# Performance work log

Hardware: AMD Instinct MI355X
Metric: run time of the kernel (lower is better)

Reference implementation:

```python
import jax, jax.numpy as jnp
import numpy as np

B = 131072
HID = 512
TEMB = 32
N_STEPS = 10


def time_embedding(t):
    # t: (B,) -> (B, TEMB) sinusoidal embedding
    half = TEMB // 2
    freqs = jnp.exp(-jnp.log(10000.0) * jnp.arange(half, dtype=jnp.float32) / half)
    args = t[:, None] * freqs[None, :]
    return jnp.concatenate([jnp.sin(args), jnp.cos(args)], axis=-1)


def setup_inputs() -> dict:
    key = jax.random.key(0)
    ks = jax.random.split(key, 9)
    def lin(k, fan_out, fan_in):
        s = 1.0 / np.sqrt(fan_in)
        kw, kb = jax.random.split(k)
        W = jax.random.uniform(kw, (fan_out, fan_in), jnp.float32, -s, s)
        b = jax.random.uniform(kb, (fan_out,), jnp.float32, -s, s)
        return W, b
    x = jax.random.normal(ks[0], (B, 2), jnp.float32)
    W0, b0 = lin(ks[1], HID, 2 + TEMB)
    W1, b1 = lin(ks[2], HID, HID)
    W2, b2 = lin(ks[3], HID, HID)
    # NOTE: original zero-inits last layer (trivial flow); use small random
    # weights so the Jacobian/log-det math is exercised non-trivially.
    W3 = 0.1 * jax.random.normal(ks[4], (2, HID), jnp.float32) / np.sqrt(HID)
    b3 = jnp.zeros((2,), jnp.float32)
    return {"x": x, "W0": W0, "b0": b0, "W1": W1, "b1": b1,
            "W2": W2, "b2": b2, "W3": W3, "b3": b3}


def reference(x, W0, b0, W1, b1, W2, b2, W3, b3):
    h_step = 1.0 / N_STEPS
    nb = x.shape[0]

    def vel(z, t):
        # z: (B,2), t: (B,) -> v: (B,2)
        h = jnp.concatenate([z, time_embedding(t)], axis=-1)
        h = jax.nn.silu(h @ W0.T + b0)
        h = jax.nn.silu(h @ W1.T + b1)
        h = jax.nn.silu(h @ W2.T + b2)
        return h @ W3.T + b3

    e0 = jnp.broadcast_to(jnp.array([1.0, 0.0], jnp.float32), (nb, 2))
    e1 = jnp.broadcast_to(jnp.array([0.0, 1.0], jnp.float32), (nb, 2))

    def step(carry, k):
        z, log_det = carry
        t = jnp.full((nb,), k * h_step, jnp.float32)
        f = lambda zz: vel(zz, t)
        # Batched JVPs give Jacobian columns: col0 = dv/dz0, col1 = dv/dz1
        v, col0 = jax.jvp(f, (z,), (e0,))
        _, col1 = jax.jvp(f, (z,), (e1,))
        det = (1.0 + h_step * col0[:, 0]) * (1.0 + h_step * col1[:, 1]) \
              - (h_step ** 2) * col1[:, 0] * col0[:, 1]
        log_det = log_det + jnp.log(jnp.clip(jnp.abs(det), 1e-8))
        z = z + h_step * v
        return (z, log_det), None

    ks = jnp.arange(N_STEPS, dtype=jnp.float32)
    (z, log_det), _ = jax.lax.scan(step, (x, jnp.zeros((nb,), jnp.float32)), ks)
    log_pz = -0.5 * jnp.sum(z ** 2 + jnp.log(2.0 * jnp.pi), axis=-1)
    return log_pz + log_det
```

## Files before the change

kernel.cpp:

```cpp
#include <hip/hip_runtime.h>
#include <hip/hip_bf16.h>
#include <math.h>


typedef float  f32x4  __attribute__((ext_vector_type(4)));
typedef float  f32x16 __attribute__((ext_vector_type(16)));
typedef __bf16 bf16x8 __attribute__((ext_vector_type(8)));

#define ROWB(r) (((r) << 10) + ((r) << 4))

static __device__ __forceinline__ unsigned pkbf2(float a, float b) {
    unsigned short lo = __builtin_bit_cast(unsigned short, __float2bfloat16(a));
    unsigned short hi = __builtin_bit_cast(unsigned short, __float2bfloat16(b));
    return (unsigned)lo | ((unsigned)hi << 16);
}

__global__ void pack_w_kernel(const float* __restrict__ W,
                              __hip_bfloat16* __restrict__ out) {
    int i  = blockIdx.x * 512 + threadIdx.x;
    int c  = i >> 13;
    int nb = (i >> 9) & 15;
    int l  = (i >> 3) & 63;
    int j  = i & 7;
    int n  = nb * 32 + (l & 31);
    int k  = c * 16 + ((l >> 5) << 3) + j;
    out[i] = __float2bfloat16(W[n * 512 + k]);
}

__global__ void pack_w0_kernel(const float* __restrict__ W0,
                               float* __restrict__ w01) {
    int o = threadIdx.x;
    w01[o * 2 + 0] = W0[o * 34 + 0];
    w01[o * 2 + 1] = W0[o * 34 + 1];
}

__global__ void cstep_kernel(const float* __restrict__ W0,
                             const float* __restrict__ b0,
                             float* __restrict__ cst) {
    int k = blockIdx.x;
    int o = threadIdx.x;
    float t = (float)k * 0.1f;
    float acc = b0[o];
    #pragma unroll
    for (int j = 0; j < 16; ++j) {
        float f   = expf(-9.210340371976184f * (float)j / 16.0f);
        float arg = t * f;
        acc += W0[o * 34 + 2 + j]  * sinf(arg);
        acc += W0[o * 34 + 18 + j] * cosf(arg);
    }
    cst[k * 512 + o] = acc;
}

__global__ __launch_bounds__(1024)
void flow_kernel(const float* __restrict__ x,
                 const float* __restrict__ w01,
                 const float* __restrict__ cst,
                 const __hip_bfloat16* __restrict__ Wpk1,
                 const __hip_bfloat16* __restrict__ Wpk2,
                 const float* __restrict__ b1,
                 const float* __restrict__ b2,
                 const float* __restrict__ W3,
                 const float* __restrict__ b3v,
                 float* __restrict__ out)
{
    __shared__ __align__(16) char Xbuf[96 * 1040];
    __shared__ float zbuf[32][2];
    __shared__ float ldbuf[32];
    __shared__ __align__(16) float part[16][32][8];

    const int tid  = threadIdx.x;
    const int lane = tid & 63;
    const int wid  = tid >> 6;
    const int l31  = lane & 31;
    const int hi   = lane >> 5;
    const int n0w  = wid << 5;
    const int wgs  = blockIdx.x << 5;

    if (tid < 32) {
        zbuf[tid][0] = x[(wgs + tid) * 2 + 0];
        zbuf[tid][1] = x[(wgs + tid) * 2 + 1];
        ldbuf[tid]   = 0.0f;
    }

    const int rowb0 = ROWB(l31);
    const int rowb1 = ROWB(32 + l31);
    const int rowb2 = ROWB(64 + l31);
    const int hi16  = hi << 4;
    const int abase = (wid << 6) + lane;
    const uint4* Wp1 = (const uint4*)Wpk1;
    const uint4* Wp2 = (const uint4*)Wpk2;

    const int s0   = tid >> 5;
    const int t32  = tid & 31;

    const char* xb = (const char*)Xbuf;

    __syncthreads();

    #pragma unroll 1
    for (int step = 0; step < 10; ++step) {
        {
            const float z0 = zbuf[s0][0];
            const float z1 = zbuf[s0][1];
            const float* cs = cst + (step << 9);
            char* base0 = Xbuf + ROWB(s0);
            #pragma unroll 1
            for (int m = 0; m < 2; ++m) {
                int ob = (t32 << 4) + (m << 3);
                const float4* wv4 = (const float4*)(w01 + (ob << 1));
                const float4* cv4 = (const float4*)(cs + ob);
                unsigned ph[4], p0[4], p1[4];
                #pragma unroll
                for (int jj = 0; jj < 4; ++jj) {
                    float4 wv = wv4[jj];
                    float4 cv = cv4[jj >> 1];
                    float c0 = (jj & 1) ? cv.z : cv.x;
                    float c1 = (jj & 1) ? cv.w : cv.y;
                    float a0  = fmaf(z0, wv.x, fmaf(z1, wv.y, c0));
                    float sg0 = 1.0f / (1.0f + __expf(-a0));
                    float h0  = a0 * sg0;
                    float sp0 = fmaf(h0, 1.0f - sg0, sg0);
                    float a1  = fmaf(z0, wv.z, fmaf(z1, wv.w, c1));
                    float sg1 = 1.0f / (1.0f + __expf(-a1));
                    float h1  = a1 * sg1;
                    float sp1 = fmaf(h1, 1.0f - sg1, sg1);
                    ph[jj] = pkbf2(h0, h1);
                    p0[jj] = pkbf2(sp0 * wv.x, sp1 * wv.z);
                    p1[jj] = pkbf2(sp0 * wv.y, sp1 * wv.w);
                }
                int off = ob << 1;
                uint4 vph = {ph[0], ph[1], ph[2], ph[3]};
                uint4 vp0 = {p0[0], p0[1], p0[2], p0[3]};
                uint4 vp1 = {p1[0], p1[1], p1[2], p1[3]};
                *(uint4*)(base0 + off)             = vph;
                *(uint4*)(base0 + ROWB(32) + off)  = vp0;
                *(uint4*)(base0 + ROWB(64) + off)  = vp1;
            }
        }
        __syncthreads();

        #pragma unroll 1
        for (int layer = 0; layer < 2; ++layer) {
            const uint4* __restrict__ Wp   = layer ? Wp2 : Wp1;
            const float* __restrict__ bias = layer ? b2  : b1;

            f32x16 acc0 = (f32x16)(0.0f);
            f32x16 acc1 = (f32x16)(0.0f);
            f32x16 acc2 = (f32x16)(0.0f);

            uint4 aCur = Wp[abase];
            #pragma unroll 2
            for (int c = 0; c < 32; ++c) {
                uint4 aNxt = Wp[abase + (((c + 1) & 31) << 10)];
                int kx = (c << 5) | hi16;
                bf16x8 bf0 = __builtin_bit_cast(bf16x8, *(const uint4*)(xb + rowb0 + kx));
                bf16x8 bf1 = __builtin_bit_cast(bf16x8, *(const uint4*)(xb + rowb1 + kx));
                bf16x8 bf2 = __builtin_bit_cast(bf16x8, *(const uint4*)(xb + rowb2 + kx));
                bf16x8 av  = __builtin_bit_cast(bf16x8, aCur);
                __builtin_amdgcn_s_setprio(1);
                acc0 = __builtin_amdgcn_mfma_f32_32x32x16_bf16(av, bf0, acc0, 0, 0, 0);
                acc1 = __builtin_amdgcn_mfma_f32_32x32x16_bf16(av, bf1, acc1, 0, 0, 0);
                acc2 = __builtin_amdgcn_mfma_f32_32x32x16_bf16(av, bf2, acc2, 0, 0, 0);
                __builtin_amdgcn_s_setprio(0);
                aCur = aNxt;
            }

            if (layer == 0) {
                __syncthreads();
                char* pb = Xbuf + ROWB(l31);
                #pragma unroll
                for (int q = 0; q < 4; ++q) {
                    int nq = n0w + 8 * q + 4 * hi;
                    f32x4 bq = *(const f32x4*)(bias + nq);
                    float hv[4], u0v[4], u1v[4];
                    #pragma unroll
                    for (int k = 0; k < 4; ++k) {
                        int reg = 4 * q + k;
                        float aa  = acc0[reg] + bq[k];
                        float sig = 1.0f / (1.0f + __expf(-aa));
                        float h   = aa * sig;
                        float sp  = fmaf(h, 1.0f - sig, sig);
                        hv[k]  = h;
                        u0v[k] = sp * acc1[reg];
                        u1v[k] = sp * acc2[reg];
                    }
                    int off = nq << 1;
                    uint2 vh = {pkbf2(hv[0],  hv[1]),  pkbf2(hv[2],  hv[3])};
                    uint2 v0 = {pkbf2(u0v[0], u0v[1]), pkbf2(u0v[2], u0v[3])};
                    uint2 v1 = {pkbf2(u1v[0], u1v[1]), pkbf2(u1v[2], u1v[3])};
                    *(uint2*)(pb + off)            = vh;
                    *(uint2*)(pb + ROWB(32) + off) = v0;
                    *(uint2*)(pb + ROWB(64) + off) = v1;
                }
                __syncthreads();
            } else {
                float q0 = 0.f, q1 = 0.f, q2 = 0.f, q3 = 0.f, q4 = 0.f, q5 = 0.f;
                #pragma unroll
                for (int q = 0; q < 4; ++q) {
                    int nq = n0w + 8 * q + 4 * hi;
                    f32x4 bq = *(const f32x4*)(bias + nq);
                    f32x4 w0 = *(const f32x4*)(W3 + nq);
                    f32x4 w1 = *(const f32x4*)(W3 + 512 + nq);
                    #pragma unroll
                    for (int k = 0; k < 4; ++k) {
                        int reg = 4 * q + k;
                        float aa  = acc0[reg] + bq[k];
                        float sig = 1.0f / (1.0f + __expf(-aa));
                        float h   = aa * sig;
                        float sp  = fmaf(h, 1.0f - sig, sig);
                        float u0  = sp * acc1[reg];
                        float u1  = sp * acc2[reg];
                        q0 = fmaf(w0[k], h,  q0);
                        q1 = fmaf(w1[k], h,  q1);
                        q2 = fmaf(w0[k], u0, q2);
                        q3 = fmaf(w1[k], u0, q3);
                        q4 = fmaf(w0[k], u1, q4);
                        q5 = fmaf(w1[k], u1, q5);
                    }
                }
                q0 += __shfl_xor(q0, 32);
                q1 += __shfl_xor(q1, 32);
                q2 += __shfl_xor(q2, 32);
                q3 += __shfl_xor(q3, 32);
                q4 += __shfl_xor(q4, 32);
                q5 += __shfl_xor(q5, 32);
                if (hi == 0) {
                    float* pp = &part[wid][l31][0];
                    pp[0] = q0; pp[1] = q1; pp[2] = q2;
                    pp[3] = q3; pp[4] = q4; pp[5] = q5;
                }
                __syncthreads();
            }
        }

        if (tid < 32) {
            float s0v = 0.f, s1v = 0.f, s2v = 0.f, s3v = 0.f, s4v = 0.f, s5v = 0.f;
            #pragma unroll
            for (int w = 0; w < 16; ++w) {
                const float* pp = &part[w][tid][0];
                f32x4 a = *(const f32x4*)(pp);
                f32x4 b = *(const f32x4*)(pp + 4);
                s0v += a[0]; s1v += a[1]; s2v += a[2];
                s3v += a[3]; s4v += b[0]; s5v += b[1];
            }
            float v0 = s0v + b3v[0];
            float v1 = s1v + b3v[1];
            float det = (1.0f + 0.1f * s2v) * (1.0f + 0.1f * s5v)
                      - 0.01f * s4v * s3v;
            ldbuf[tid] += logf(fmaxf(fabsf(det), 1e-8f));
            zbuf[tid][0] += 0.1f * v0;
            zbuf[tid][1] += 0.1f * v1;
        }
        __syncthreads();
    }

    if (tid < 32) {
        float z0 = zbuf[tid][0], z1 = zbuf[tid][1];
        out[wgs + tid] = -0.5f * (z0 * z0 + z1 * z1) - 1.8378770664093453f + ldbuf[tid];
    }
}

extern "C" void kernel_launch(void* const* d_in, const int* in_sizes, int n_in,
                              void* d_out, int out_size, void* d_ws, size_t ws_size,
                              hipStream_t stream) {
    const float* x  = (const float*)d_in[0];
    const float* W0 = (const float*)d_in[1];
    const float* b0 = (const float*)d_in[2];
    const float* W1 = (const float*)d_in[3];
    const float* b1 = (const float*)d_in[4];
    const float* W2 = (const float*)d_in[5];
    const float* b2 = (const float*)d_in[6];
    const float* W3 = (const float*)d_in[7];
    const float* b3 = (const float*)d_in[8];
    float* out = (float*)d_out;

    char* ws = (char*)d_ws;
    __hip_bfloat16* wpk1 = (__hip_bfloat16*)ws;
    __hip_bfloat16* wpk2 = (__hip_bfloat16*)(ws + (512u << 10));
    float*          cstp = (float*)(ws + (1024u << 10));
    float*          w01p = (float*)(ws + (1044u << 10));

    pack_w_kernel<<<512, 512, 0, stream>>>(W1, wpk1);
    pack_w_kernel<<<512, 512, 0, stream>>>(W2, wpk2);
    cstep_kernel<<<10, 512, 0, stream>>>(W0, b0, cstp);
    pack_w0_kernel<<<1, 512, 0, stream>>>(W0, w01p);
    flow_kernel<<<131072 / 32, 1024, 0, stream>>>(x, w01p, cstp, wpk1, wpk2,
                                                  b1, b2, W3, b3, out);
}
```

Before: 5.215 ms.

## Halve block to 8 waves, each computing two 32-wide output tiles

The flow kernel now launches 512 threads (8 waves) per block instead of 1024. Each wave computes two 32-column output tiles per layer, reusing each B fragment read from LDS for two MFMAs and doubling the accumulator count. The first-layer prologue, epilogues and partial-sum reduction are adjusted to match. This aims to cut LDS reads per MFMA and per-block synchronisation overhead, at the cost of higher register pressure (six 16-float accumulators) and fewer waves available to hide latency.

```diff
diff --git a/kernel.cpp b/kernel.cpp
--- a/kernel.cpp
+++ b/kernel.cpp
@@ -51,7 +51,7 @@
     cst[k * 512 + o] = acc;
 }
 
-__global__ __launch_bounds__(1024)
+__global__ __launch_bounds__(512)
 void flow_kernel(const float* __restrict__ x,
                  const float* __restrict__ w01,
                  const float* __restrict__ cst,
@@ -66,14 +66,14 @@
     __shared__ __align__(16) char Xbuf[96 * 1040];
     __shared__ float zbuf[32][2];
     __shared__ float ldbuf[32];
-    __shared__ __align__(16) float part[16][32][8];
+    __shared__ __align__(16) float part[8][32][8];
 
     const int tid  = threadIdx.x;
     const int lane = tid & 63;
     const int wid  = tid >> 6;
     const int l31  = lane & 31;
     const int hi   = lane >> 5;
-    const int n0w  = wid << 5;
+    const int n0w  = wid << 6;
     const int wgs  = blockIdx.x << 5;
 
     if (tid < 32) {
@@ -86,12 +86,12 @@
     const int rowb1 = ROWB(32 + l31);
     const int rowb2 = ROWB(64 + l31);
     const int hi16  = hi << 4;
-    const int abase = (wid << 6) + lane;
+    const int abase = (wid << 7) + lane;
     const uint4* Wp1 = (const uint4*)Wpk1;
     const uint4* Wp2 = (const uint4*)Wpk2;
 
-    const int s0   = tid >> 5;
-    const int t32  = tid & 31;
+    const int s0  = tid >> 4;
+    const int t16 = tid & 15;
 
     const char* xb = (const char*)Xbuf;
 
@@ -105,8 +105,8 @@
             const float* cs = cst + (step << 9);
             char* base0 = Xbuf + ROWB(s0);
             #pragma unroll 1
-            for (int m = 0; m < 2; ++m) {
-                int ob = (t32 << 4) + (m << 3);
+            for (int m = 0; m < 4; ++m) {
+                int ob = (t16 << 5) + (m << 3);
                 const float4* wv4 = (const float4*)(w01 + (ob << 1));
                 const float4* cv4 = (const float4*)(cs + ob);
                 unsigned ph[4], p0[4], p1[4];
@@ -144,78 +144,97 @@
             const uint4* __restrict__ Wp   = layer ? Wp2 : Wp1;
             const float* __restrict__ bias = layer ? b2  : b1;
 
-            f32x16 acc0 = (f32x16)(0.0f);
-            f32x16 acc1 = (f32x16)(0.0f);
-            f32x16 acc2 = (f32x16)(0.0f);
-
-            uint4 aCur = Wp[abase];
+            f32x16 acc00 = (f32x16)(0.0f), acc01 = (f32x16)(0.0f), acc02 = (f32x16)(0.0f);
+            f32x16 acc10 = (f32x16)(0.0f), acc11 = (f32x16)(0.0f), acc12 = (f32x16)(0.0f);
+
+            uint4 aCur0 = Wp[abase];
+            uint4 aCur1 = Wp[abase + 64];
             #pragma unroll 2
             for (int c = 0; c < 32; ++c) {
-                uint4 aNxt = Wp[abase + (((c + 1) & 31) << 10)];
+                int nidx = abase + (((c + 1) & 31) << 10);
+                uint4 aNxt0 = Wp[nidx];
+                uint4 aNxt1 = Wp[nidx + 64];
                 int kx = (c << 5) | hi16;
                 bf16x8 bf0 = __builtin_bit_cast(bf16x8, *(const uint4*)(xb + rowb0 + kx));
                 bf16x8 bf1 = __builtin_bit_cast(bf16x8, *(const uint4*)(xb + rowb1 + kx));
                 bf16x8 bf2 = __builtin_bit_cast(bf16x8, *(const uint4*)(xb + rowb2 + kx));
-                bf16x8 av  = __builtin_bit_cast(bf16x8, aCur);
+                bf16x8 av0 = __builtin_bit_cast(bf16x8, aCur0);
+                bf16x8 av1 = __builtin_bit_cast(bf16x8, aCur1);
                 __builtin_amdgcn_s_setprio(1);
-                acc0 = __builtin_amdgcn_mfma_f32_32x32x16_bf16(av, bf0, acc0, 0, 0, 0);
-                acc1 = __builtin_amdgcn_mfma_f32_32x32x16_bf16(av, bf1, acc1, 0, 0, 0);
-                acc2 = __builtin_amdgcn_mfma_f32_32x32x16_bf16(av, bf2, acc2, 0, 0, 0);
+                acc00 = __builtin_amdgcn_mfma_f32_32x32x16_bf16(av0, bf0, acc00, 0, 0, 0);
+                acc10 = __builtin_amdgcn_mfma_f32_32x32x16_bf16(av1, bf0, acc10, 0, 0, 0);
+                acc01 = __builtin_amdgcn_mfma_f32_32x32x16_bf16(av0, bf1, acc01, 0, 0, 0);
+                acc11 = __builtin_amdgcn_mfma_f32_32x32x16_bf16(av1, bf1, acc11, 0, 0, 0);
+                acc02 = __builtin_amdgcn_mfma_f32_32x32x16_bf16(av0, bf2, acc02, 0, 0, 0);
+                acc12 = __builtin_amdgcn_mfma_f32_32x32x16_bf16(av1, bf2, acc12, 0, 0, 0);
                 __builtin_amdgcn_s_setprio(0);
-                aCur = aNxt;
+                aCur0 = aNxt0;
+                aCur1 = aNxt1;
             }
 
             if (layer == 0) {
                 __syncthreads();
                 char* pb = Xbuf + ROWB(l31);
                 #pragma unroll
-                for (int q = 0; q < 4; ++q) {
-                    int nq = n0w + 8 * q + 4 * hi;
-                    f32x4 bq = *(const f32x4*)(bias + nq);
-                    float hv[4], u0v[4], u1v[4];
+                for (int nt = 0; nt < 2; ++nt) {
+                    const f32x16& a0r = nt ? acc10 : acc00;
+                    const f32x16& a1r = nt ? acc11 : acc01;
+                    const f32x16& a2r = nt ? acc12 : acc02;
                     #pragma unroll
-                    for (int k = 0; k < 4; ++k) {
-                        int reg = 4 * q + k;
-                        float aa  = acc0[reg] + bq[k];
-                        float sig = 1.0f / (1.0f + __expf(-aa));
-                        float h   = aa * sig;
-                        float sp  = fmaf(h, 1.0f - sig, sig);
-                        hv[k]  = h;
-                        u0v[k] = sp * acc1[reg];
-                        u1v[k] = sp * acc2[reg];
+                    for (int q = 0; q < 4; ++q) {
+                        int nq = n0w + nt * 32 + 8 * q + 4 * hi;
+                        f32x4 bq = *(const f32x4*)(bias + nq);
+                        float hv[4], u0v[4], u1v[4];
+                        #pragma unroll
+                        for (int k = 0; k < 4; ++k) {
+                            int reg = 4 * q + k;
+                            float aa  = a0r[reg] + bq[k];
+                            float sig = 1.0f / (1.0f + __expf(-aa));
+                            float h   = aa * sig;
+                            float sp  = fmaf(h, 1.0f - sig, sig);
+                            hv[k]  = h;
+                            u0v[k] = sp * a1r[reg];
+                            u1v[k] = sp * a2r[reg];
+                        }
+                        int off = nq << 1;
+                        uint2 vh = {pkbf2(hv[0],  hv[1]),  pkbf2(hv[2],  hv[3])};
+                        uint2 v0 = {pkbf2(u0v[0], u0v[1]), pkbf2(u0v[2], u0v[3])};
+                        uint2 v1 = {pkbf2(u1v[0], u1v[1]), pkbf2(u1v[2], u1v[3])};
+                        *(uint2*)(pb + off)            = vh;
+                        *(uint2*)(pb + ROWB(32) + off) = v0;
+                        *(uint2*)(pb + ROWB(64) + off) = v1;
                     }
-                    int off = nq << 1;
-                    uint2 vh = {pkbf2(hv[0],  hv[1]),  pkbf2(hv[2],  hv[3])};
-                    uint2 v0 = {pkbf2(u0v[0], u0v[1]), pkbf2(u0v[2], u0v[3])};
-                    uint2 v1 = {pkbf2(u1v[0], u1v[1]), pkbf2(u1v[2], u1v[3])};
-                    *(uint2*)(pb + off)            = vh;
-                    *(uint2*)(pb + ROWB(32) + off) = v0;
-                    *(uint2*)(pb + ROWB(64) + off) = v1;
                 }
                 __syncthreads();
             } else {
                 float q0 = 0.f, q1 = 0.f, q2 = 0.f, q3 = 0.f, q4 = 0.f, q5 = 0.f;
                 #pragma unroll
-                for (int q = 0; q < 4; ++q) {
-                    int nq = n0w + 8 * q + 4 * hi;
-                    f32x4 bq = *(const f32x4*)(bias + nq);
-                    f32x4 w0 = *(const f32x4*)(W3 + nq);
-                    f32x4 w1 = *(const f32x4*)(W3 + 512 + nq);
+                for (int nt = 0; nt < 2; ++nt) {
+                    const f32x16& a0r = nt ? acc10 : acc00;
+                    const f32x16& a1r = nt ? acc11 : acc01;
+                    const f32x16& a2r = nt ? acc12 : acc02;
                     #pragma unroll
-                    for (int k = 0; k < 4; ++k) {
-                        int reg = 4 * q + k;
-                        float aa  = acc0[reg] + bq[k];
-                        float sig = 1.0f / (1.0f + __expf(-aa));
-                        float h   = aa * sig;
-                        float sp  = fmaf(h, 1.0f - sig, sig);
-                        float u0  = sp * acc1[reg];
-                        float u1  = sp * acc2[reg];
-                        q0 = fmaf(w0[k], h,  q0);
-                        q1 = fmaf(w1[k], h,  q1);
-                        q2 = fmaf(w0[k], u0, q2);
-                        q3 = fmaf(w1[k], u0, q3);
-                        q4 = fmaf(w0[k], u1, q4);
-                        q5 = fmaf(w1[k], u1, q5);
+                    for (int q = 0; q < 4; ++q) {
+                        int nq = n0w + nt * 32 + 8 * q + 4 * hi;
+                        f32x4 bq = *(const f32x4*)(bias + nq);
+                        f32x4 w0 = *(const f32x4*)(W3 + nq);
+                        f32x4 w1 = *(const f32x4*)(W3 + 512 + nq);
+                        #pragma unroll
+                        for (int k = 0; k < 4; ++k) {
+                            int reg = 4 * q + k;
+                            float aa  = a0r[reg] + bq[k];
+                            float sig = 1.0f / (1.0f + __expf(-aa));
+                            float h   = aa * sig;
+                            float sp  = fmaf(h, 1.0f - sig, sig);
+                            float u0  = sp * a1r[reg];
+                            float u1  = sp * a2r[reg];
+                            q0 = fmaf(w0[k], h,  q0);
+                            q1 = fmaf(w1[k], h,  q1);
+                            q2 = fmaf(w0[k], u0, q2);
+                            q3 = fmaf(w1[k], u0, q3);
+                            q4 = fmaf(w0[k], u1, q4);
+                            q5 = fmaf(w1[k], u1, q5);
+                        }
                     }
                 }
                 q0 += __shfl_xor(q0, 32);
@@ -236,7 +255,7 @@
         if (tid < 32) {
             float s0v = 0.f, s1v = 0.f, s2v = 0.f, s3v = 0.f, s4v = 0.f, s5v = 0.f;
             #pragma unroll
-            for (int w = 0; w < 16; ++w) {
+            for (int w = 0; w < 8; ++w) {
                 const float* pp = &part[w][tid][0];
                 f32x4 a = *(const f32x4*)(pp);
                 f32x4 b = *(const f32x4*)(pp + 4);
@@ -284,6 +303,6 @@
     pack_w_kernel<<<512, 512, 0, stream>>>(W2, wpk2);
     cstep_kernel<<<10, 512, 0, stream>>>(W0, b0, cstp);
     pack_w0_kernel<<<1, 512, 0, stream>>>(W0, w01p);
-    flow_kernel<<<131072 / 32, 1024, 0, stream>>>(x, w01p, cstp, wpk1, wpk2,
-                                                  b1, b2, W3, b3, out);
-}
+    flow_kernel<<<131072 / 32, 512, 0, stream>>>(x, w01p, cstp, wpk1, wpk2,
+                                                 b1, b2, W3, b3, out);
+}
```

Measured after the change: 4.951 ms. 5.1% less time.
